# Kernel tuning notes

Measured on AMD Instinct MI355X. Metric: run time of the kernel, lower is better.

Reference implementation:

```python
import jax, jax.numpy as jnp
import numpy as np

B, H, N, C, E, D, L_OUT, LAYERS = 16, 64, 512, 3, 128, 32, 12, 2


def setup_inputs() -> dict:
    key = jax.random.key(0)
    ks = jax.random.split(key, 16)
    nrm = lambda k, s, sc=1.0: jax.random.normal(k, s, jnp.float32) * sc
    adj = jax.random.uniform(ks[0], (N, N), jnp.float32)
    adj = adj / adj.sum(axis=-1, keepdims=True)  # row-normalized prior adjacency
    return {
        "x_input": nrm(ks[1], (B, H, N, C)),
        "adj": adj,
        "Wf": nrm(ks[2], (3, E, 3 * C), 0.1),
        "Uf": nrm(ks[3], (3, E, E), 0.05),
        "bf": jnp.zeros((3, E), jnp.float32),
        "E1f": nrm(ks[4], (N, D)),
        "E2f": nrm(ks[5], (N, D)),
        "Wb": nrm(ks[6], (3, E, 3 * C), 0.1),
        "Ub": nrm(ks[7], (3, E, E), 0.05),
        "bb": jnp.zeros((3, E), jnp.float32),
        "E1b": nrm(ks[8], (N, D)),
        "E2b": nrm(ks[9], (N, D)),
        "dec_w": nrm(ks[10], (L_OUT, LAYERS, 2 * E), 0.05),  # Conv2d(layer_num->out_len, k=(1,2E)) squeezed
        "dec_b": jnp.zeros((L_OUT,), jnp.float32),
        "out_w": nrm(ks[11], (L_OUT, L_OUT), 0.1),  # 1x1 Conv2d squeezed
        "out_b": jnp.zeros((L_OUT,), jnp.float32),
    }


def _cell_step(c, xt, adj, A_dyn, W, U, b):
    # Graph-coupled GRU cell (IBNCell): xt [B,C,N], c [B,E,N].
    msg = jnp.concatenate(
        [xt,
         jnp.einsum('bcn,nm->bcm', xt, adj),      # prior-graph message passing
         jnp.einsum('bcn,nm->bcm', xt, A_dyn)],   # learned dynamic-graph message passing
        axis=1)  # [B, 3C, N]
    gx = jnp.einsum('goc,bcn->gbon', W, msg)  # 3 stacked gate projections
    r = jax.nn.sigmoid(gx[0] + jnp.einsum('oe,ben->bon', U[0], c) + b[0][:, None])
    u = jax.nn.sigmoid(gx[1] + jnp.einsum('oe,ben->bon', U[1], c) + b[1][:, None])
    g = jnp.tanh(gx[2] + jnp.einsum('oe,ben->bon', U[2], r * c) + b[2][:, None])
    return u * c + (1.0 - u) * g


def _forward(x_input, adj, Wf, Uf, bf, E1f, E2f, Wb, Ub, bb, E1b, E2b, dec_w, dec_b, out_w, out_b):
    # torch: x_input.transpose(-3,-1).transpose(-2,-1) -> [B,C,H,N]; scan layout [H,B,C,N]
    xs = jnp.transpose(x_input, (1, 0, 3, 2))
    A_f = jax.nn.softmax(jax.nn.relu(E1f @ E2f.T), axis=-1)  # dynamic adjacency, fwd cell
    A_b = jax.nn.softmax(jax.nn.relu(E1b @ E2b.T), axis=-1)  # dynamic adjacency, back cell
    c0 = jnp.zeros((xs.shape[1], Wf.shape[1], xs.shape[3]), xs.dtype)  # [B,E,N]

    def step_f(c, xt):
        cn = _cell_step(c, xt, adj, A_f, Wf, Uf, bf)
        return cn, None

    # Output only depends on the last timestep of the bidirectional concat:
    # forward branch -> final state after H steps; backward branch (after flip)
    # at t=H-1 -> its FIRST step (input x[H-1]). Dead per-step outputs elided.
    h_fwd, _ = jax.lax.scan(step_f, c0, xs)
    h_back0 = _cell_step(c0, xs[-1], adj, A_b, Wb, Ub, bb)
    last_ht = jnp.concatenate([h_fwd, h_back0], axis=1)  # [B, 2E, N]

    lt = jnp.transpose(last_ht, (0, 2, 1))  # [B, N, 2E]
    # layer loop z>0 is a no-op on current_layer_output -> final_result repeats last_ht
    final = jnp.broadcast_to(lt[:, None], (lt.shape[0], LAYERS, lt.shape[1], lt.shape[2]))
    h = jnp.einsum('blne,ole->bon', final, dec_w) + dec_b[:, None]  # decoder conv (1,2E)
    return jnp.einsum('oi,bin->bon', out_w, h) + out_b[:, None]  # 1x1 output conv -> [B,L_OUT,N]


def reference(x_input, adj, Wf, Uf, bf, E1f, E2f, Wb, Ub, bb, E1b, E2b, dec_w, dec_b, out_w, out_b):
    return _forward(x_input, adj, Wf, Uf, bf, E1f, E2f, Wb, Ub, bb, E1b, E2b, dec_w, dec_b, out_w, out_b)
```

## Files before the change

### kernel.cpp

```cpp
#include <hip/hip_runtime.h>


typedef _Float16 half8_t __attribute__((ext_vector_type(8)));
typedef __fp16 fp16x2_t __attribute__((ext_vector_type(2)));
typedef float float4_t __attribute__((ext_vector_type(4)));

#define PIN(x) asm volatile("" : "+v"(x))

__device__ __forceinline__ float exp2_(float x) { return __builtin_amdgcn_exp2f(x); }
__device__ __forceinline__ float rcp_(float x) { return __builtin_amdgcn_rcpf(x); }

__global__ __launch_bounds__(256) void prep_kernel(
    const float* __restrict__ E1f, const float* __restrict__ E2f,
    const float* __restrict__ E1b, const float* __restrict__ E2b,
    const float* __restrict__ adj, const float* __restrict__ Wf,
    const float* __restrict__ Uf, const float* __restrict__ bf,
    const float* __restrict__ Wb, const float* __restrict__ bb,
    _Float16* __restrict__ adjT, _Float16* __restrict__ AfT,
    _Float16* __restrict__ AbT, _Float16* __restrict__ ufrag,
    _Float16* __restrict__ wbfrag, _Float16* __restrict__ zpad) {
  int bid = blockIdx.x;
  int tid = threadIdx.x;
  if (bid >= 1288) {
    if (tid < 64) zpad[tid] = (_Float16)0.f;
    return;
  }
  if (bid >= 1272) {
    int r2 = bid - 1272;
    int gi = 1 + (r2 & 1);
    int og = r2 >> 1;
    float scl = (gi == 2) ? 2.8853902f : -1.4426950f;
    for (int e = tid; e < 512; e += 256) {
      int lane = e >> 3, j = e & 7;
      int o = og * 16 + (lane & 15);
      int q = (lane >> 4) * 8 + j;
      float v = (q < 9) ? Wb[gi * 1152 + o * 9 + q]
                        : (q == 9 ? bb[gi * 128 + o] : 0.f);
      wbfrag[r2 * 512 + e] = (_Float16)(v * scl);
    }
    return;
  }
  if (bid >= 1152) {
    int r = bid - 1152;
    int kb = r % 5;
    int gi = (r / 5) % 3;
    int og = r / 15;
    float scl = (gi == 2) ? 2.8853902f : -1.4426950f;
    for (int e = tid; e < 512; e += 256) {
      int lane = e >> 3, j = e & 7;
      int o = og * 16 + (lane & 15);
      int q4 = lane >> 4;
      float v;
      if (kb < 4) {
        v = Uf[gi * 16384 + o * 128 + kb * 32 + q4 * 8 + j];
      } else {
        int q = q4 * 8 + j;
        v = (q < 9) ? Wf[gi * 1152 + o * 9 + q]
                    : (q == 9 ? bf[gi * 128 + o] : 0.f);
      }
      ufrag[r * 512 + e] = (_Float16)(v * scl);
    }
    return;
  }
  if (bid >= 1024) {
    int base = (bid - 1024) * 4;
    for (int r = 0; r < 4; ++r) {
      int row = base + r;
      float v0 = adj[row * 512 + tid];
      float v1 = adj[row * 512 + tid + 256];
      adjT[(size_t)tid * 512 + row] = (_Float16)v0;
      adjT[(size_t)(tid + 256) * 512 + row] = (_Float16)v1;
    }
    return;
  }
  int which = bid >> 9;
  int row = bid & 511;
  const float* E1 = which ? E1b : E1f;
  const float* E2 = which ? E2b : E2f;
  _Float16* A = which ? AbT : AfT;
  __shared__ float e1s[32];
  __shared__ float red[256];
  if (tid < 32) e1s[tid] = E1[row * 32 + tid];
  __syncthreads();
  float s[2];
#pragma unroll
  for (int h = 0; h < 2; ++h) {
    int m = tid + h * 256;
    const float4* e2 = (const float4*)(E2 + m * 32);
    float acc = 0.f;
#pragma unroll
    for (int d4 = 0; d4 < 8; ++d4) {
      float4 v = e2[d4];
      acc = fmaf(v.x, e1s[d4 * 4 + 0], acc);
      acc = fmaf(v.y, e1s[d4 * 4 + 1], acc);
      acc = fmaf(v.z, e1s[d4 * 4 + 2], acc);
      acc = fmaf(v.w, e1s[d4 * 4 + 3], acc);
    }
    s[h] = fmaxf(acc, 0.f);
  }
  red[tid] = fmaxf(s[0], s[1]);
  __syncthreads();
  for (int off = 128; off > 0; off >>= 1) {
    if (tid < off) red[tid] = fmaxf(red[tid], red[tid + off]);
    __syncthreads();
  }
  float mx = red[0];
  __syncthreads();
  float e0 = __expf(s[0] - mx), e1v = __expf(s[1] - mx);
  red[tid] = e0 + e1v;
  __syncthreads();
  for (int off = 128; off > 0; off >>= 1) {
    if (tid < off) red[tid] += red[tid + off];
    __syncthreads();
  }
  float inv = rcp_(red[0]);
  A[(size_t)tid * 512 + row] = (_Float16)(e0 * inv);
  A[(size_t)(tid + 256) * 512 + row] = (_Float16)(e1v * inv);
}

__global__ __launch_bounds__(256, 2) void msg_kernel(
    const float* __restrict__ x, const _Float16* __restrict__ adjT,
    const _Float16* __restrict__ AfT, const _Float16* __restrict__ AbT,
    _Float16* __restrict__ msg16, _Float16* __restrict__ msgb16) {
  __shared__ __align__(16) _Float16 Alds[48 * 512];
  __shared__ __align__(16) _Float16 Sst[1024 * 16];
  int tid = threadIdx.x;
  int t = blockIdx.x >> 3;
  int n0g = (blockIdx.x & 7) * 64;
  int lane = tid & 63, og = tid >> 6;
  int l15 = lane & 15, q4 = lane >> 4, q0 = q4 * 8;
  bool is63 = (t == 63);

  {
    int b = tid >> 4, li = tid & 15;
    const float4* xb = (const float4*)(x + (size_t)(b * 64 + t) * 1536);
#pragma unroll
    for (int k = 0; k < 24; ++k) {
      float4 v = xb[k * 16 + li];
      int j0 = (k * 16 + li) * 4;
#pragma unroll
      for (int e = 0; e < 4; ++e) {
        int j = j0 + e;
        int n = (j * 21846) >> 16;
        int c = j - n * 3;
        int m = b * 3 + c;
        float val = (e == 0) ? v.x : (e == 1) ? v.y : (e == 2) ? v.z : v.w;
        Alds[m * 512 + ((((n >> 3) ^ (m & 7)) << 3) | (n & 7))] = (_Float16)val;
      }
    }
  }
  __syncthreads();

  const float4_t zero4 = {0.f, 0.f, 0.f, 0.f};
  float4_t acc[3][2], accb[3];
#pragma unroll
  for (int mt = 0; mt < 3; ++mt) { acc[mt][0] = zero4; acc[mt][1] = zero4; accb[mt] = zero4; }

  int n = n0g + og * 16 + l15;
  for (int kb = 0; kb < 16; ++kb) {
    half8_t afr[3];
#pragma unroll
    for (int mt = 0; mt < 3; ++mt) {
      int m = mt * 16 + l15;
      afr[mt] = *(const half8_t*)&Alds[m * 512 + ((((kb * 4 + q4) ^ (m & 7)) << 3))];
    }
    half8_t b0 = *(const half8_t*)&adjT[(size_t)n * 512 + kb * 32 + q0];
    half8_t b1 = *(const half8_t*)&AfT[(size_t)n * 512 + kb * 32 + q0];
#pragma unroll
    for (int mt = 0; mt < 3; ++mt) {
      acc[mt][0] = __builtin_amdgcn_mfma_f32_16x16x32_f16(afr[mt], b0, acc[mt][0], 0, 0, 0);
      acc[mt][1] = __builtin_amdgcn_mfma_f32_16x16x32_f16(afr[mt], b1, acc[mt][1], 0, 0, 0);
    }
    if (is63) {
      half8_t b2 = *(const half8_t*)&AbT[(size_t)n * 512 + kb * 32 + q0];
#pragma unroll
      for (int mt = 0; mt < 3; ++mt)
        accb[mt] = __builtin_amdgcn_mfma_f32_16x16x32_f16(afr[mt], b2, accb[mt], 0, 0, 0);
    }
  }

  for (int i = tid; i < 1024; i += 256) {
    int tb = i >> 6, nl = i & 63;
    int nn = n0g + nl;
    _Float16* row = &Sst[i * 16];
#pragma unroll
    for (int c = 0; c < 3; ++c) {
      int m = tb * 3 + c;
      row[c] = Alds[m * 512 + ((((nn >> 3) ^ (m & 7)) << 3) | (nn & 7))];
    }
    row[9] = (_Float16)1.f;
#pragma unroll
    for (int z = 10; z < 16; ++z) row[z] = (_Float16)0.f;
  }
#pragma unroll
  for (int mt = 0; mt < 3; ++mt)
#pragma unroll
    for (int r = 0; r < 4; ++r) {
      int m = mt * 16 + q4 * 4 + r;
      int tb = (m * 21846) >> 16;
      int c = m - tb * 3;
      _Float16* row = &Sst[(tb * 64 + og * 16 + l15) * 16];
      row[3 + c] = (_Float16)acc[mt][0][r];
      row[6 + c] = (_Float16)acc[mt][1][r];
    }
  __syncthreads();
  for (int i = tid; i < 2048; i += 256) {
    int rrow = i >> 1, h = i & 1;
    int tb = rrow >> 6, nl = rrow & 63;
    ((uint4*)msg16)[(((size_t)(t * 16 + tb) * 512) + n0g + nl) * 2 + h] =
        ((const uint4*)Sst)[i];
  }
  if (is63) {
    __syncthreads();
#pragma unroll
    for (int mt = 0; mt < 3; ++mt)
#pragma unroll
      for (int r = 0; r < 4; ++r) {
        int m = mt * 16 + q4 * 4 + r;
        int tb = (m * 21846) >> 16;
        int c = m - tb * 3;
        Sst[(tb * 64 + og * 16 + l15) * 16 + 6 + c] = (_Float16)accb[mt][r];
      }
    __syncthreads();
    for (int i = tid; i < 2048; i += 256) {
      int rrow = i >> 1, h = i & 1;
      int tb = rrow >> 6, nl = rrow & 63;
      ((uint4*)msgb16)[(((size_t)tb * 512) + n0g + nl) * 2 + h] =
          ((const uint4*)Sst)[i];
    }
  }
}

__global__ __launch_bounds__(512, 4) void rec_kernel(
    const _Float16* __restrict__ msg16, const _Float16* __restrict__ msgb16,
    const _Float16* __restrict__ zpad, const _Float16* __restrict__ ufrag,
    const _Float16* __restrict__ wbfrag, const float* __restrict__ dec_w,
    const float* __restrict__ dec_b, const float* __restrict__ out_w,
    const float* __restrict__ out_b, float* __restrict__ out) {
  __shared__ __align__(16) _Float16 Cbuf[2048];
  __shared__ __align__(16) _Float16 Gbuf[2048];
  __shared__ float hf_lds[128 * 16];
  __shared__ float hb_lds[128 * 16];
  __shared__ float hdec_lds[12 * 16];
  int tid = threadIdx.x, bid = blockIdx.x;
  int b = bid >> 5;
  int nt = bid & 31;
  int n0 = nt * 16;
  int lane = tid & 63, og = tid >> 6;
  int l15 = lane & 15, q4 = lane >> 4;

  half8_t afrag[3][5];
#pragma unroll
  for (int gi = 0; gi < 3; ++gi)
#pragma unroll
    for (int kb = 0; kb < 5; ++kb) {
      afrag[gi][kb] = *(const half8_t*)
          &ufrag[(size_t)(((og * 3 + gi) * 5 + kb) * 512) + lane * 8];
      PIN(afrag[gi][kb]);
    }

  if (tid < 256) {
    uint4 z; z.x = z.y = z.z = z.w = 0;
    ((uint4*)Cbuf)[tid] = z;
  }
  float cr[4] = {0.f, 0.f, 0.f, 0.f};

  const float4_t zero4 = {0.f, 0.f, 0.f, 0.f};
  union H4U { fp16x2_t h2[2]; unsigned long long u; };
  const char* base = (const char*)msg16 +
                     ((size_t)(b * 512 + n0 + l15)) * 32 + (q4 & 1) * 16;
  const char* pcur = (q4 < 2) ? base : (const char*)zpad;
  size_t tstr = (q4 < 2) ? (size_t)16 * 512 * 32 : 0;

  half8_t bm0 = *(const half8_t*)pcur;
  float4_t accr_p = __builtin_amdgcn_mfma_f32_16x16x32_f16(afrag[0][4], bm0, zero4, 0, 0, 0);
  float4_t accu_p = __builtin_amdgcn_mfma_f32_16x16x32_f16(afrag[1][4], bm0, zero4, 0, 0, 0);
  float4_t accg_p = __builtin_amdgcn_mfma_f32_16x16x32_f16(afrag[2][4], bm0, zero4, 0, 0, 0);

  int kb_w = og >> 1;
  int lane_w = ((og & 1) * 2 + (q4 >> 1)) * 16 + l15;
  int j0 = (q4 & 1) * 4;
  __syncthreads();

  for (int t = 0; t < 64; ++t) {
    const char* pnext = pcur + tstr;
    half8_t bm_n = *(const half8_t*)pnext;

    half8_t cf[4];
#pragma unroll
    for (int kb = 0; kb < 4; ++kb)
      cf[kb] = *(const half8_t*)&Cbuf[(kb * 64 + lane) * 8];

    float4_t accr = accr_p, accu = accu_p;
    __builtin_amdgcn_s_setprio(1);
#pragma unroll
    for (int kb = 0; kb < 4; ++kb) {
      accr = __builtin_amdgcn_mfma_f32_16x16x32_f16(afrag[0][kb], cf[kb], accr, 0, 0, 0);
      accu = __builtin_amdgcn_mfma_f32_16x16x32_f16(afrag[1][kb], cf[kb], accu, 0, 0, 0);
    }
    __builtin_amdgcn_s_setprio(0);

    float Eu[4];
    {
      H4U v;
#pragma unroll
      for (int r = 0; r < 2; ++r) {
        float a = rcp_(1.f + exp2_(accr[2 * r])) * cr[2 * r];
        float bq = rcp_(1.f + exp2_(accr[2 * r + 1])) * cr[2 * r + 1];
        v.h2[r] = __builtin_amdgcn_cvt_pkrtz(a, bq);
      }
      *(unsigned long long*)&Gbuf[(kb_w * 64 + lane_w) * 8 + j0] = v.u;
#pragma unroll
      for (int r = 0; r < 4; ++r) Eu[r] = exp2_(accu[r]);
    }
    __syncthreads();

    half8_t gf[4];
#pragma unroll
    for (int kb = 0; kb < 4; ++kb)
      gf[kb] = *(const half8_t*)&Gbuf[(kb * 64 + lane) * 8];
    float4_t accg = accg_p;
    __builtin_amdgcn_s_setprio(1);
#pragma unroll
    for (int kb = 0; kb < 4; ++kb)
      accg = __builtin_amdgcn_mfma_f32_16x16x32_f16(afrag[2][kb], gf[kb], accg, 0, 0, 0);
    __builtin_amdgcn_s_setprio(0);

    {
      H4U v;
      float cn[4];
#pragma unroll
      for (int r = 0; r < 4; ++r) {
        float Eg = exp2_(accg[r]);
        float d0 = Eg + 1.f;
        float den = fmaf(Eu[r], d0, d0);
        float num = fmaf(cr[r], Eg, cr[r]) + fmaf(Eu[r], Eg, -Eu[r]);
        cn[r] = num * rcp_(den);
        cr[r] = cn[r];
      }
      v.h2[0] = __builtin_amdgcn_cvt_pkrtz(cn[0], cn[1]);
      v.h2[1] = __builtin_amdgcn_cvt_pkrtz(cn[2], cn[3]);
      *(unsigned long long*)&Cbuf[(kb_w * 64 + lane_w) * 8 + j0] = v.u;
    }
    accr_p = __builtin_amdgcn_mfma_f32_16x16x32_f16(afrag[0][4], bm_n, zero4, 0, 0, 0);
    accu_p = __builtin_amdgcn_mfma_f32_16x16x32_f16(afrag[1][4], bm_n, zero4, 0, 0, 0);
    accg_p = __builtin_amdgcn_mfma_f32_16x16x32_f16(afrag[2][4], bm_n, zero4, 0, 0, 0);
    __syncthreads();
    pcur = pnext;
  }

  {
    const char* bb_base = (const char*)msgb16 +
                          ((size_t)(b * 512 + n0 + l15)) * 32 + (q4 & 1) * 16;
    const char* bp = (q4 < 2) ? bb_base : (const char*)zpad;
    half8_t bbk = *(const half8_t*)bp;
    half8_t au_f = *(const half8_t*)&wbfrag[(size_t)((og * 2 + 0) * 512) + lane * 8];
    half8_t ag_f = *(const half8_t*)&wbfrag[(size_t)((og * 2 + 1) * 512) + lane * 8];
    float4_t au = __builtin_amdgcn_mfma_f32_16x16x32_f16(au_f, bbk, zero4, 0, 0, 0);
    float4_t ag = __builtin_amdgcn_mfma_f32_16x16x32_f16(ag_f, bbk, zero4, 0, 0, 0);
#pragma unroll
    for (int r = 0; r < 4; ++r) {
      int row = og * 16 + q4 * 4 + r;
      float uu2 = rcp_(1.f + exp2_(au[r]));
      float gg = fmaf(-2.f, rcp_(exp2_(ag[r]) + 1.f), 1.f);
      hb_lds[row * 16 + l15] = (1.f - uu2) * gg;
      hf_lds[row * 16 + l15] = cr[r];
    }
  }
  __syncthreads();

  if (tid < 192) {
    int i = tid >> 4, cc = tid & 15;
    const float* dwa = dec_w + (size_t)i * 512;
    const float* dwb = dwa + 256;
    float hd = dec_b[i];
    for (int e = 0; e < 128; ++e) {
      hd = fmaf(dwa[e] + dwb[e], hf_lds[e * 16 + cc], hd);
      hd = fmaf(dwa[128 + e] + dwb[128 + e], hb_lds[e * 16 + cc], hd);
    }
    hdec_lds[i * 16 + cc] = hd;
  }
  __syncthreads();
  if (tid < 192) {
    int o = tid >> 4, cc = tid & 15;
    float v = out_b[o];
#pragma unroll
    for (int i = 0; i < 12; ++i) v = fmaf(out_w[o * 12 + i], hdec_lds[i * 16 + cc], v);
    out[((size_t)(b * 12 + o)) * 512 + n0 + cc] = v;
  }
}

extern "C" void kernel_launch(void* const* d_in, const int* in_sizes, int n_in,
                              void* d_out, int out_size, void* d_ws, size_t ws_size,
                              hipStream_t stream) {
  (void)in_sizes; (void)n_in; (void)out_size; (void)ws_size;
  const float* x     = (const float*)d_in[0];
  const float* adj   = (const float*)d_in[1];
  const float* Wf    = (const float*)d_in[2];
  const float* Uf    = (const float*)d_in[3];
  const float* bf    = (const float*)d_in[4];
  const float* E1f   = (const float*)d_in[5];
  const float* E2f   = (const float*)d_in[6];
  const float* Wb    = (const float*)d_in[7];
  const float* bb    = (const float*)d_in[9];
  const float* E1b   = (const float*)d_in[10];
  const float* E2b   = (const float*)d_in[11];
  const float* dec_w = (const float*)d_in[12];
  const float* dec_b = (const float*)d_in[13];
  const float* out_w = (const float*)d_in[14];
  const float* out_b = (const float*)d_in[15];

  _Float16* h      = (_Float16*)d_ws;
  _Float16* adjT   = h;
  _Float16* AfT    = h + 262144;
  _Float16* AbT    = h + 524288;
  _Float16* ufrag  = h + 786432;
  _Float16* wbfrag = h + 847872;
  _Float16* zpad   = h + 856064;
  _Float16* msg16  = h + 856128;
  _Float16* msgb16 = h + 9244736;

  prep_kernel<<<1289, 256, 0, stream>>>(E1f, E2f, E1b, E2b, adj, Wf, Uf, bf,
                                        Wb, bb, adjT, AfT, AbT, ufrag, wbfrag, zpad);
  msg_kernel<<<512, 256, 0, stream>>>(x, adjT, AfT, AbT, msg16, msgb16);
  rec_kernel<<<512, 512, 0, stream>>>(msg16, msgb16, zpad, ufrag, wbfrag,
                                      dec_w, dec_b, out_w, out_b, (float*)d_out);
}
```

Measured before the change: 198.4 us.

## Process two independent node tiles per block in recurrent kernel for ILP

Each rec_kernel block now handles two 16-node tiles (P and Q) at once, with duplicated LDS state buffers and interleaved MFMA chains, and the grid is halved to 256 blocks. The aim is to hide MFMA and transcendental latency in the serial 64-step recurrence by interleaving two independent dependency chains, and to amortise the per-step barriers and the register-held weight fragments over twice the work. In exchange the block count drops to 256, which on a 256-CU part leaves one block per CU, and register and LDS pressure rises (launch bounds relaxed to 2 blocks per CU). The input-projection MFMAs are also moved from the previous iteration's tail into the current step.

```diff
diff --git a/kernel.cpp b/kernel.cpp
--- a/kernel.cpp
+++ b/kernel.cpp
@@ -231,21 +231,22 @@
   }
 }
 
-__global__ __launch_bounds__(512, 4) void rec_kernel(
+__global__ __launch_bounds__(512, 2) void rec_kernel(
     const _Float16* __restrict__ msg16, const _Float16* __restrict__ msgb16,
     const _Float16* __restrict__ zpad, const _Float16* __restrict__ ufrag,
     const _Float16* __restrict__ wbfrag, const float* __restrict__ dec_w,
     const float* __restrict__ dec_b, const float* __restrict__ out_w,
     const float* __restrict__ out_b, float* __restrict__ out) {
-  __shared__ __align__(16) _Float16 Cbuf[2048];
-  __shared__ __align__(16) _Float16 Gbuf[2048];
-  __shared__ float hf_lds[128 * 16];
-  __shared__ float hb_lds[128 * 16];
-  __shared__ float hdec_lds[12 * 16];
+  __shared__ __align__(16) _Float16 CbufP[2048];
+  __shared__ __align__(16) _Float16 GbufP[2048];
+  __shared__ __align__(16) _Float16 CbufQ[2048];
+  __shared__ __align__(16) _Float16 GbufQ[2048];
+  __shared__ float hfP[128 * 16], hbP[128 * 16];
+  __shared__ float hfQ[128 * 16], hbQ[128 * 16];
+  __shared__ float hdecP[192], hdecQ[192];
   int tid = threadIdx.x, bid = blockIdx.x;
-  int b = bid >> 5;
-  int nt = bid & 31;
-  int n0 = nt * 16;
+  int b = bid >> 4;
+  int n0 = (bid & 15) * 32;
   int lane = tid & 63, og = tid >> 6;
   int l15 = lane & 15, q4 = lane >> 4;
 
@@ -259,23 +260,23 @@
       PIN(afrag[gi][kb]);
     }
 
-  if (tid < 256) {
+  {
     uint4 z; z.x = z.y = z.z = z.w = 0;
-    ((uint4*)Cbuf)[tid] = z;
-  }
-  float cr[4] = {0.f, 0.f, 0.f, 0.f};
+    if (tid < 256) ((uint4*)CbufP)[tid] = z;
+    else ((uint4*)CbufQ)[tid - 256] = z;
+  }
+  float crP[4] = {0.f, 0.f, 0.f, 0.f};
+  float crQ[4] = {0.f, 0.f, 0.f, 0.f};
 
   const float4_t zero4 = {0.f, 0.f, 0.f, 0.f};
   union H4U { fp16x2_t h2[2]; unsigned long long u; };
-  const char* base = (const char*)msg16 +
-                     ((size_t)(b * 512 + n0 + l15)) * 32 + (q4 & 1) * 16;
-  const char* pcur = (q4 < 2) ? base : (const char*)zpad;
+  const char* baseP = (const char*)msg16 +
+                      ((size_t)(b * 512 + n0 + l15)) * 32 + (q4 & 1) * 16;
+  const char* pcurP = (q4 < 2) ? baseP : (const char*)zpad;
+  const char* pcurQ = (q4 < 2) ? (baseP + 16 * 32) : (const char*)zpad;
   size_t tstr = (q4 < 2) ? (size_t)16 * 512 * 32 : 0;
-
-  half8_t bm0 = *(const half8_t*)pcur;
-  float4_t accr_p = __builtin_amdgcn_mfma_f32_16x16x32_f16(afrag[0][4], bm0, zero4, 0, 0, 0);
-  float4_t accu_p = __builtin_amdgcn_mfma_f32_16x16x32_f16(afrag[1][4], bm0, zero4, 0, 0, 0);
-  float4_t accg_p = __builtin_amdgcn_mfma_f32_16x16x32_f16(afrag[2][4], bm0, zero4, 0, 0, 0);
+  half8_t bmP = *(const half8_t*)pcurP;
+  half8_t bmQ = *(const half8_t*)pcurQ;
 
   int kb_w = og >> 1;
   int lane_w = ((og & 1) * 2 + (q4 >> 1)) * 16 + l15;
@@ -283,88 +284,132 @@
   __syncthreads();
 
   for (int t = 0; t < 64; ++t) {
-    const char* pnext = pcur + tstr;
-    half8_t bm_n = *(const half8_t*)pnext;
-
-    half8_t cf[4];
-#pragma unroll
-    for (int kb = 0; kb < 4; ++kb)
-      cf[kb] = *(const half8_t*)&Cbuf[(kb * 64 + lane) * 8];
-
-    float4_t accr = accr_p, accu = accu_p;
+    const char* pnP = pcurP + tstr;
+    const char* pnQ = pcurQ + tstr;
+    half8_t bmPn = *(const half8_t*)pnP;
+    half8_t bmQn = *(const half8_t*)pnQ;
+
+    half8_t cfP[4], cfQ[4];
+#pragma unroll
+    for (int kb = 0; kb < 4; ++kb) {
+      cfP[kb] = *(const half8_t*)&CbufP[(kb * 64 + lane) * 8];
+      cfQ[kb] = *(const half8_t*)&CbufQ[(kb * 64 + lane) * 8];
+    }
+
+    float4_t accrP = __builtin_amdgcn_mfma_f32_16x16x32_f16(afrag[0][4], bmP, zero4, 0, 0, 0);
+    float4_t accuP = __builtin_amdgcn_mfma_f32_16x16x32_f16(afrag[1][4], bmP, zero4, 0, 0, 0);
+    float4_t accrQ = __builtin_amdgcn_mfma_f32_16x16x32_f16(afrag[0][4], bmQ, zero4, 0, 0, 0);
+    float4_t accuQ = __builtin_amdgcn_mfma_f32_16x16x32_f16(afrag[1][4], bmQ, zero4, 0, 0, 0);
     __builtin_amdgcn_s_setprio(1);
 #pragma unroll
     for (int kb = 0; kb < 4; ++kb) {
-      accr = __builtin_amdgcn_mfma_f32_16x16x32_f16(afrag[0][kb], cf[kb], accr, 0, 0, 0);
-      accu = __builtin_amdgcn_mfma_f32_16x16x32_f16(afrag[1][kb], cf[kb], accu, 0, 0, 0);
+      accrP = __builtin_amdgcn_mfma_f32_16x16x32_f16(afrag[0][kb], cfP[kb], accrP, 0, 0, 0);
+      accrQ = __builtin_amdgcn_mfma_f32_16x16x32_f16(afrag[0][kb], cfQ[kb], accrQ, 0, 0, 0);
+      accuP = __builtin_amdgcn_mfma_f32_16x16x32_f16(afrag[1][kb], cfP[kb], accuP, 0, 0, 0);
+      accuQ = __builtin_amdgcn_mfma_f32_16x16x32_f16(afrag[1][kb], cfQ[kb], accuQ, 0, 0, 0);
     }
     __builtin_amdgcn_s_setprio(0);
 
-    float Eu[4];
+    float EuP[4], EuQ[4];
     {
       H4U v;
 #pragma unroll
       for (int r = 0; r < 2; ++r) {
-        float a = rcp_(1.f + exp2_(accr[2 * r])) * cr[2 * r];
-        float bq = rcp_(1.f + exp2_(accr[2 * r + 1])) * cr[2 * r + 1];
+        float a = rcp_(1.f + exp2_(accrP[2 * r])) * crP[2 * r];
+        float bq = rcp_(1.f + exp2_(accrP[2 * r + 1])) * crP[2 * r + 1];
         v.h2[r] = __builtin_amdgcn_cvt_pkrtz(a, bq);
       }
-      *(unsigned long long*)&Gbuf[(kb_w * 64 + lane_w) * 8 + j0] = v.u;
-#pragma unroll
-      for (int r = 0; r < 4; ++r) Eu[r] = exp2_(accu[r]);
-    }
-    __syncthreads();
-
-    half8_t gf[4];
-#pragma unroll
-    for (int kb = 0; kb < 4; ++kb)
-      gf[kb] = *(const half8_t*)&Gbuf[(kb * 64 + lane) * 8];
-    float4_t accg = accg_p;
+      *(unsigned long long*)&GbufP[(kb_w * 64 + lane_w) * 8 + j0] = v.u;
+      H4U w;
+#pragma unroll
+      for (int r = 0; r < 2; ++r) {
+        float a = rcp_(1.f + exp2_(accrQ[2 * r])) * crQ[2 * r];
+        float bq = rcp_(1.f + exp2_(accrQ[2 * r + 1])) * crQ[2 * r + 1];
+        w.h2[r] = __builtin_amdgcn_cvt_pkrtz(a, bq);
+      }
+      *(unsigned long long*)&GbufQ[(kb_w * 64 + lane_w) * 8 + j0] = w.u;
+#pragma unroll
+      for (int r = 0; r < 4; ++r) {
+        EuP[r] = exp2_(accuP[r]);
+        EuQ[r] = exp2_(accuQ[r]);
+      }
+    }
+    __syncthreads();
+
+    half8_t gfP[4], gfQ[4];
+#pragma unroll
+    for (int kb = 0; kb < 4; ++kb) {
+      gfP[kb] = *(const half8_t*)&GbufP[(kb * 64 + lane) * 8];
+      gfQ[kb] = *(const half8_t*)&GbufQ[(kb * 64 + lane) * 8];
+    }
+    float4_t accgP = __builtin_amdgcn_mfma_f32_16x16x32_f16(afrag[2][4], bmP, zero4, 0, 0, 0);
+    float4_t accgQ = __builtin_amdgcn_mfma_f32_16x16x32_f16(afrag[2][4], bmQ, zero4, 0, 0, 0);
     __builtin_amdgcn_s_setprio(1);
 #pragma unroll
-    for (int kb = 0; kb < 4; ++kb)
-      accg = __builtin_amdgcn_mfma_f32_16x16x32_f16(afrag[2][kb], gf[kb], accg, 0, 0, 0);
+    for (int kb = 0; kb < 4; ++kb) {
+      accgP = __builtin_amdgcn_mfma_f32_16x16x32_f16(afrag[2][kb], gfP[kb], accgP, 0, 0, 0);
+      accgQ = __builtin_amdgcn_mfma_f32_16x16x32_f16(afrag[2][kb], gfQ[kb], accgQ, 0, 0, 0);
+    }
     __builtin_amdgcn_s_setprio(0);
 
     {
       H4U v;
-      float cn[4];
+      float cnP[4], cnQ[4];
 #pragma unroll
       for (int r = 0; r < 4; ++r) {
-        float Eg = exp2_(accg[r]);
+        float Eg = exp2_(accgP[r]);
         float d0 = Eg + 1.f;
-        float den = fmaf(Eu[r], d0, d0);
-        float num = fmaf(cr[r], Eg, cr[r]) + fmaf(Eu[r], Eg, -Eu[r]);
-        cn[r] = num * rcp_(den);
-        cr[r] = cn[r];
-      }
-      v.h2[0] = __builtin_amdgcn_cvt_pkrtz(cn[0], cn[1]);
-      v.h2[1] = __builtin_amdgcn_cvt_pkrtz(cn[2], cn[3]);
-      *(unsigned long long*)&Cbuf[(kb_w * 64 + lane_w) * 8 + j0] = v.u;
-    }
-    accr_p = __builtin_amdgcn_mfma_f32_16x16x32_f16(afrag[0][4], bm_n, zero4, 0, 0, 0);
-    accu_p = __builtin_amdgcn_mfma_f32_16x16x32_f16(afrag[1][4], bm_n, zero4, 0, 0, 0);
-    accg_p = __builtin_amdgcn_mfma_f32_16x16x32_f16(afrag[2][4], bm_n, zero4, 0, 0, 0);
-    __syncthreads();
-    pcur = pnext;
+        float den = fmaf(EuP[r], d0, d0);
+        float num = fmaf(crP[r], Eg, crP[r]) + fmaf(EuP[r], Eg, -EuP[r]);
+        cnP[r] = num * rcp_(den);
+        crP[r] = cnP[r];
+      }
+      v.h2[0] = __builtin_amdgcn_cvt_pkrtz(cnP[0], cnP[1]);
+      v.h2[1] = __builtin_amdgcn_cvt_pkrtz(cnP[2], cnP[3]);
+      *(unsigned long long*)&CbufP[(kb_w * 64 + lane_w) * 8 + j0] = v.u;
+      H4U w;
+#pragma unroll
+      for (int r = 0; r < 4; ++r) {
+        float Eg = exp2_(accgQ[r]);
+        float d0 = Eg + 1.f;
+        float den = fmaf(EuQ[r], d0, d0);
+        float num = fmaf(crQ[r], Eg, crQ[r]) + fmaf(EuQ[r], Eg, -EuQ[r]);
+        cnQ[r] = num * rcp_(den);
+        crQ[r] = cnQ[r];
+      }
+      w.h2[0] = __builtin_amdgcn_cvt_pkrtz(cnQ[0], cnQ[1]);
+      w.h2[1] = __builtin_amdgcn_cvt_pkrtz(cnQ[2], cnQ[3]);
+      *(unsigned long long*)&CbufQ[(kb_w * 64 + lane_w) * 8 + j0] = w.u;
+    }
+    __syncthreads();
+    bmP = bmPn; bmQ = bmQn;
+    pcurP = pnP; pcurQ = pnQ;
   }
 
   {
-    const char* bb_base = (const char*)msgb16 +
-                          ((size_t)(b * 512 + n0 + l15)) * 32 + (q4 & 1) * 16;
-    const char* bp = (q4 < 2) ? bb_base : (const char*)zpad;
-    half8_t bbk = *(const half8_t*)bp;
+    const char* bbP = (const char*)msgb16 +
+                      ((size_t)(b * 512 + n0 + l15)) * 32 + (q4 & 1) * 16;
+    const char* bpP = (q4 < 2) ? bbP : (const char*)zpad;
+    const char* bpQ = (q4 < 2) ? (bbP + 16 * 32) : (const char*)zpad;
+    half8_t bkP = *(const half8_t*)bpP;
+    half8_t bkQ = *(const half8_t*)bpQ;
     half8_t au_f = *(const half8_t*)&wbfrag[(size_t)((og * 2 + 0) * 512) + lane * 8];
     half8_t ag_f = *(const half8_t*)&wbfrag[(size_t)((og * 2 + 1) * 512) + lane * 8];
-    float4_t au = __builtin_amdgcn_mfma_f32_16x16x32_f16(au_f, bbk, zero4, 0, 0, 0);
-    float4_t ag = __builtin_amdgcn_mfma_f32_16x16x32_f16(ag_f, bbk, zero4, 0, 0, 0);
+    float4_t auP = __builtin_amdgcn_mfma_f32_16x16x32_f16(au_f, bkP, zero4, 0, 0, 0);
+    float4_t agP = __builtin_amdgcn_mfma_f32_16x16x32_f16(ag_f, bkP, zero4, 0, 0, 0);
+    float4_t auQ = __builtin_amdgcn_mfma_f32_16x16x32_f16(au_f, bkQ, zero4, 0, 0, 0);
+    float4_t agQ = __builtin_amdgcn_mfma_f32_16x16x32_f16(ag_f, bkQ, zero4, 0, 0, 0);
 #pragma unroll
     for (int r = 0; r < 4; ++r) {
       int row = og * 16 + q4 * 4 + r;
-      float uu2 = rcp_(1.f + exp2_(au[r]));
-      float gg = fmaf(-2.f, rcp_(exp2_(ag[r]) + 1.f), 1.f);
-      hb_lds[row * 16 + l15] = (1.f - uu2) * gg;
-      hf_lds[row * 16 + l15] = cr[r];
+      float uuP = rcp_(1.f + exp2_(auP[r]));
+      float ggP = fmaf(-2.f, rcp_(exp2_(agP[r]) + 1.f), 1.f);
+      hbP[row * 16 + l15] = (1.f - uuP) * ggP;
+      hfP[row * 16 + l15] = crP[r];
+      float uuQ = rcp_(1.f + exp2_(auQ[r]));
+      float ggQ = fmaf(-2.f, rcp_(exp2_(agQ[r]) + 1.f), 1.f);
+      hbQ[row * 16 + l15] = (1.f - uuQ) * ggQ;
+      hfQ[row * 16 + l15] = crQ[r];
     }
   }
   __syncthreads();
@@ -375,18 +420,36 @@
     const float* dwb = dwa + 256;
     float hd = dec_b[i];
     for (int e = 0; e < 128; ++e) {
-      hd = fmaf(dwa[e] + dwb[e], hf_lds[e * 16 + cc], hd);
-      hd = fmaf(dwa[128 + e] + dwb[128 + e], hb_lds[e * 16 + cc], hd);
-    }
-    hdec_lds[i * 16 + cc] = hd;
+      hd = fmaf(dwa[e] + dwb[e], hfP[e * 16 + cc], hd);
+      hd = fmaf(dwa[128 + e] + dwb[128 + e], hbP[e * 16 + cc], hd);
+    }
+    hdecP[i * 16 + cc] = hd;
+  } else if (tid >= 256 && tid < 448) {
+    int t2 = tid - 256;
+    int i = t2 >> 4, cc = t2 & 15;
+    const float* dwa = dec_w + (size_t)i * 512;
+    const float* dwb = dwa + 256;
+    float hd = dec_b[i];
+    for (int e = 0; e < 128; ++e) {
+      hd = fmaf(dwa[e] + dwb[e], hfQ[e * 16 + cc], hd);
+      hd = fmaf(dwa[128 + e] + dwb[128 + e], hbQ[e * 16 + cc], hd);
+    }
+    hdecQ[i * 16 + cc] = hd;
   }
   __syncthreads();
   if (tid < 192) {
     int o = tid >> 4, cc = tid & 15;
     float v = out_b[o];
 #pragma unroll
-    for (int i = 0; i < 12; ++i) v = fmaf(out_w[o * 12 + i], hdec_lds[i * 16 + cc], v);
+    for (int i = 0; i < 12; ++i) v = fmaf(out_w[o * 12 + i], hdecP[i * 16 + cc], v);
     out[((size_t)(b * 12 + o)) * 512 + n0 + cc] = v;
+  } else if (tid >= 256 && tid < 448) {
+    int t2 = tid - 256;
+    int o = t2 >> 4, cc = t2 & 15;
+    float v = out_b[o];
+#pragma unroll
+    for (int i = 0; i < 12; ++i) v = fmaf(out_w[o * 12 + i], hdecQ[i * 16 + cc], v);
+    out[((size_t)(b * 12 + o)) * 512 + n0 + 16 + cc] = v;
   }
 }
 
@@ -423,6 +486,6 @@
   prep_kernel<<<1289, 256, 0, stream>>>(E1f, E2f, E1b, E2b, adj, Wf, Uf, bf,
                                         Wb, bb, adjT, AfT, AbT, ufrag, wbfrag, zpad);
   msg_kernel<<<512, 256, 0, stream>>>(x, adjT, AfT, AbT, msg16, msgb16);
-  rec_kernel<<<512, 512, 0, stream>>>(msg16, msgb16, zpad, ufrag, wbfrag,
+  rec_kernel<<<256, 512, 0, stream>>>(msg16, msgb16, zpad, ufrag, wbfrag,
                                       dec_w, dec_b, out_w, out_b, (float*)d_out);
 }
```

New measurement: 209.0 us. +5.4%, slower.

## Halve rec_kernel waves so each wave computes two interleaved gate row tiles

Applied to the files above, without the earlier changes.

The recurrent kernel now runs 4 waves of 256 threads instead of 8. Each wave owns two 16-row output tiles and interleaves their independent MFMA chains, which is meant to hide MFMA latency and make the per-step barriers cheaper. The input-projection MFMAs are no longer precomputed for the next step; they now start each step's accumulation. That adds work on the serial critical path and roughly doubles the VGPRs pinned for weight fragments.

```diff
diff --git a/kernel.cpp b/kernel.cpp
--- a/kernel.cpp
+++ b/kernel.cpp
@@ -231,7 +231,7 @@
   }
 }
 
-__global__ __launch_bounds__(512, 4) void rec_kernel(
+__global__ __launch_bounds__(256, 2) void rec_kernel(
     const _Float16* __restrict__ msg16, const _Float16* __restrict__ msgb16,
     const _Float16* __restrict__ zpad, const _Float16* __restrict__ ufrag,
     const _Float16* __restrict__ wbfrag, const float* __restrict__ dec_w,
@@ -249,21 +249,23 @@
   int lane = tid & 63, og = tid >> 6;
   int l15 = lane & 15, q4 = lane >> 4;
 
-  half8_t afrag[3][5];
-#pragma unroll
-  for (int gi = 0; gi < 3; ++gi)
-#pragma unroll
-    for (int kb = 0; kb < 5; ++kb) {
-      afrag[gi][kb] = *(const half8_t*)
-          &ufrag[(size_t)(((og * 3 + gi) * 5 + kb) * 512) + lane * 8];
-      PIN(afrag[gi][kb]);
-    }
-
-  if (tid < 256) {
+  half8_t afrag[2][3][5];
+#pragma unroll
+  for (int h = 0; h < 2; ++h)
+#pragma unroll
+    for (int gi = 0; gi < 3; ++gi)
+#pragma unroll
+      for (int kb = 0; kb < 5; ++kb) {
+        afrag[h][gi][kb] = *(const half8_t*)
+            &ufrag[(size_t)((((og * 2 + h) * 3 + gi) * 5 + kb) * 512) + lane * 8];
+        PIN(afrag[h][gi][kb]);
+      }
+
+  {
     uint4 z; z.x = z.y = z.z = z.w = 0;
     ((uint4*)Cbuf)[tid] = z;
   }
-  float cr[4] = {0.f, 0.f, 0.f, 0.f};
+  float cr[2][4] = {{0.f, 0.f, 0.f, 0.f}, {0.f, 0.f, 0.f, 0.f}};
 
   const float4_t zero4 = {0.f, 0.f, 0.f, 0.f};
   union H4U { fp16x2_t h2[2]; unsigned long long u; };
@@ -271,15 +273,10 @@
                      ((size_t)(b * 512 + n0 + l15)) * 32 + (q4 & 1) * 16;
   const char* pcur = (q4 < 2) ? base : (const char*)zpad;
   size_t tstr = (q4 < 2) ? (size_t)16 * 512 * 32 : 0;
-
-  half8_t bm0 = *(const half8_t*)pcur;
-  float4_t accr_p = __builtin_amdgcn_mfma_f32_16x16x32_f16(afrag[0][4], bm0, zero4, 0, 0, 0);
-  float4_t accu_p = __builtin_amdgcn_mfma_f32_16x16x32_f16(afrag[1][4], bm0, zero4, 0, 0, 0);
-  float4_t accg_p = __builtin_amdgcn_mfma_f32_16x16x32_f16(afrag[2][4], bm0, zero4, 0, 0, 0);
-
-  int kb_w = og >> 1;
-  int lane_w = ((og & 1) * 2 + (q4 >> 1)) * 16 + l15;
+  half8_t bm = *(const half8_t*)pcur;
+
   int j0 = (q4 & 1) * 4;
+  int lwbase = (q4 >> 1) * 16 + l15;
   __syncthreads();
 
   for (int t = 0; t < 64; ++t) {
@@ -291,27 +288,35 @@
     for (int kb = 0; kb < 4; ++kb)
       cf[kb] = *(const half8_t*)&Cbuf[(kb * 64 + lane) * 8];
 
-    float4_t accr = accr_p, accu = accu_p;
+    float4_t accr[2], accu[2];
     __builtin_amdgcn_s_setprio(1);
 #pragma unroll
-    for (int kb = 0; kb < 4; ++kb) {
-      accr = __builtin_amdgcn_mfma_f32_16x16x32_f16(afrag[0][kb], cf[kb], accr, 0, 0, 0);
-      accu = __builtin_amdgcn_mfma_f32_16x16x32_f16(afrag[1][kb], cf[kb], accu, 0, 0, 0);
-    }
+    for (int h = 0; h < 2; ++h) {
+      accr[h] = __builtin_amdgcn_mfma_f32_16x16x32_f16(afrag[h][0][4], bm, zero4, 0, 0, 0);
+      accu[h] = __builtin_amdgcn_mfma_f32_16x16x32_f16(afrag[h][1][4], bm, zero4, 0, 0, 0);
+    }
+#pragma unroll
+    for (int kb = 0; kb < 4; ++kb)
+#pragma unroll
+      for (int h = 0; h < 2; ++h) {
+        accr[h] = __builtin_amdgcn_mfma_f32_16x16x32_f16(afrag[h][0][kb], cf[kb], accr[h], 0, 0, 0);
+        accu[h] = __builtin_amdgcn_mfma_f32_16x16x32_f16(afrag[h][1][kb], cf[kb], accu[h], 0, 0, 0);
+      }
     __builtin_amdgcn_s_setprio(0);
 
-    float Eu[4];
-    {
+    float Eu[2][4];
+#pragma unroll
+    for (int h = 0; h < 2; ++h) {
       H4U v;
 #pragma unroll
       for (int r = 0; r < 2; ++r) {
-        float a = rcp_(1.f + exp2_(accr[2 * r])) * cr[2 * r];
-        float bq = rcp_(1.f + exp2_(accr[2 * r + 1])) * cr[2 * r + 1];
+        float a = rcp_(1.f + exp2_(accr[h][2 * r])) * cr[h][2 * r];
+        float bq = rcp_(1.f + exp2_(accr[h][2 * r + 1])) * cr[h][2 * r + 1];
         v.h2[r] = __builtin_amdgcn_cvt_pkrtz(a, bq);
       }
-      *(unsigned long long*)&Gbuf[(kb_w * 64 + lane_w) * 8 + j0] = v.u;
-#pragma unroll
-      for (int r = 0; r < 4; ++r) Eu[r] = exp2_(accu[r]);
+      *(unsigned long long*)&Gbuf[(og * 64 + h * 32 + lwbase) * 8 + j0] = v.u;
+#pragma unroll
+      for (int r = 0; r < 4; ++r) Eu[h][r] = exp2_(accu[h][r]);
     }
     __syncthreads();
 
@@ -319,33 +324,37 @@
 #pragma unroll
     for (int kb = 0; kb < 4; ++kb)
       gf[kb] = *(const half8_t*)&Gbuf[(kb * 64 + lane) * 8];
-    float4_t accg = accg_p;
+    float4_t accg[2];
     __builtin_amdgcn_s_setprio(1);
 #pragma unroll
+    for (int h = 0; h < 2; ++h)
+      accg[h] = __builtin_amdgcn_mfma_f32_16x16x32_f16(afrag[h][2][4], bm, zero4, 0, 0, 0);
+#pragma unroll
     for (int kb = 0; kb < 4; ++kb)
-      accg = __builtin_amdgcn_mfma_f32_16x16x32_f16(afrag[2][kb], gf[kb], accg, 0, 0, 0);
+#pragma unroll
+      for (int h = 0; h < 2; ++h)
+        accg[h] = __builtin_amdgcn_mfma_f32_16x16x32_f16(afrag[h][2][kb], gf[kb], accg[h], 0, 0, 0);
     __builtin_amdgcn_s_setprio(0);
 
-    {
+#pragma unroll
+    for (int h = 0; h < 2; ++h) {
       H4U v;
       float cn[4];
 #pragma unroll
       for (int r = 0; r < 4; ++r) {
-        float Eg = exp2_(accg[r]);
+        float Eg = exp2_(accg[h][r]);
         float d0 = Eg + 1.f;
-        float den = fmaf(Eu[r], d0, d0);
-        float num = fmaf(cr[r], Eg, cr[r]) + fmaf(Eu[r], Eg, -Eu[r]);
+        float den = fmaf(Eu[h][r], d0, d0);
+        float num = fmaf(cr[h][r], Eg, cr[h][r]) + fmaf(Eu[h][r], Eg, -Eu[h][r]);
         cn[r] = num * rcp_(den);
-        cr[r] = cn[r];
+        cr[h][r] = cn[r];
       }
       v.h2[0] = __builtin_amdgcn_cvt_pkrtz(cn[0], cn[1]);
       v.h2[1] = __builtin_amdgcn_cvt_pkrtz(cn[2], cn[3]);
-      *(unsigned long long*)&Cbuf[(kb_w * 64 + lane_w) * 8 + j0] = v.u;
-    }
-    accr_p = __builtin_amdgcn_mfma_f32_16x16x32_f16(afrag[0][4], bm_n, zero4, 0, 0, 0);
-    accu_p = __builtin_amdgcn_mfma_f32_16x16x32_f16(afrag[1][4], bm_n, zero4, 0, 0, 0);
-    accg_p = __builtin_amdgcn_mfma_f32_16x16x32_f16(afrag[2][4], bm_n, zero4, 0, 0, 0);
-    __syncthreads();
+      *(unsigned long long*)&Cbuf[(og * 64 + h * 32 + lwbase) * 8 + j0] = v.u;
+    }
+    __syncthreads();
+    bm = bm_n;
     pcur = pnext;
   }
 
@@ -354,17 +363,21 @@
                           ((size_t)(b * 512 + n0 + l15)) * 32 + (q4 & 1) * 16;
     const char* bp = (q4 < 2) ? bb_base : (const char*)zpad;
     half8_t bbk = *(const half8_t*)bp;
-    half8_t au_f = *(const half8_t*)&wbfrag[(size_t)((og * 2 + 0) * 512) + lane * 8];
-    half8_t ag_f = *(const half8_t*)&wbfrag[(size_t)((og * 2 + 1) * 512) + lane * 8];
-    float4_t au = __builtin_amdgcn_mfma_f32_16x16x32_f16(au_f, bbk, zero4, 0, 0, 0);
-    float4_t ag = __builtin_amdgcn_mfma_f32_16x16x32_f16(ag_f, bbk, zero4, 0, 0, 0);
-#pragma unroll
-    for (int r = 0; r < 4; ++r) {
-      int row = og * 16 + q4 * 4 + r;
-      float uu2 = rcp_(1.f + exp2_(au[r]));
-      float gg = fmaf(-2.f, rcp_(exp2_(ag[r]) + 1.f), 1.f);
-      hb_lds[row * 16 + l15] = (1.f - uu2) * gg;
-      hf_lds[row * 16 + l15] = cr[r];
+#pragma unroll
+    for (int h = 0; h < 2; ++h) {
+      int oo = og * 2 + h;
+      half8_t au_f = *(const half8_t*)&wbfrag[(size_t)((oo * 2 + 0) * 512) + lane * 8];
+      half8_t ag_f = *(const half8_t*)&wbfrag[(size_t)((oo * 2 + 1) * 512) + lane * 8];
+      float4_t au = __builtin_amdgcn_mfma_f32_16x16x32_f16(au_f, bbk, zero4, 0, 0, 0);
+      float4_t ag = __builtin_amdgcn_mfma_f32_16x16x32_f16(ag_f, bbk, zero4, 0, 0, 0);
+#pragma unroll
+      for (int r = 0; r < 4; ++r) {
+        int row = oo * 16 + q4 * 4 + r;
+        float uu2 = rcp_(1.f + exp2_(au[r]));
+        float gg = fmaf(-2.f, rcp_(exp2_(ag[r]) + 1.f), 1.f);
+        hb_lds[row * 16 + l15] = (1.f - uu2) * gg;
+        hf_lds[row * 16 + l15] = cr[h][r];
+      }
     }
   }
   __syncthreads();
@@ -423,6 +436,6 @@
   prep_kernel<<<1289, 256, 0, stream>>>(E1f, E2f, E1b, E2b, adj, Wf, Uf, bf,
                                         Wb, bb, adjT, AfT, AbT, ufrag, wbfrag, zpad);
   msg_kernel<<<512, 256, 0, stream>>>(x, adjT, AfT, AbT, msg16, msgb16);
-  rec_kernel<<<512, 512, 0, stream>>>(msg16, msgb16, zpad, ufrag, wbfrag,
+  rec_kernel<<<512, 256, 0, stream>>>(msg16, msgb16, zpad, ufrag, wbfrag,
                                       dec_w, dec_b, out_w, out_b, (float*)d_out);
 }
```

Result: slower. 203.7 us (+2.7%).

## Move update-gate MFMAs off the critical path and vectorize x staging

Applied to the files above, without the earlier changes.

In the recurrent scan, the update-gate (u) matmul and its input projection now run after the first barrier, alongside the candidate-gate MFMAs, so only the reset gate sits before the first synchronization. The intent is to shorten the serialized path between the C load and the G write and barrier. In exchange the phase after the barrier carries more MFMA work and bm must stay live across iterations. Separately, msg_kernel's x staging now loads 24 contiguous floats per thread, packs them to fp16 pairs and writes 16-byte LDS stores instead of scalar half stores with divide-by-3 indexing.

```diff
diff --git a/kernel.cpp b/kernel.cpp
--- a/kernel.cpp
+++ b/kernel.cpp
@@ -132,20 +132,24 @@
   bool is63 = (t == 63);
 
   {
-    int b = tid >> 4, li = tid & 15;
-    const float4* xb = (const float4*)(x + (size_t)(b * 64 + t) * 1536);
-#pragma unroll
-    for (int k = 0; k < 24; ++k) {
-      float4 v = xb[k * 16 + li];
-      int j0 = (k * 16 + li) * 4;
-#pragma unroll
-      for (int e = 0; e < 4; ++e) {
-        int j = j0 + e;
-        int n = (j * 21846) >> 16;
-        int c = j - n * 3;
+    union F24 { float4 v4[6]; float f[24]; };
+    union P16 { fp16x2_t h2[4]; uint4 u; };
+#pragma unroll
+    for (int it = 0; it < 4; ++it) {
+      int task = tid + it * 256;
+      int b = task >> 6, chunk = task & 63;
+      F24 fv;
+      const float4* xb4 = (const float4*)x + ((size_t)(b * 64 + t) * 384 + chunk * 6);
+#pragma unroll
+      for (int i = 0; i < 6; ++i) fv.v4[i] = xb4[i];
+#pragma unroll
+      for (int c = 0; c < 3; ++c) {
+        P16 p;
+#pragma unroll
+        for (int i = 0; i < 4; ++i)
+          p.h2[i] = __builtin_amdgcn_cvt_pkrtz(fv.f[6 * i + c], fv.f[6 * i + 3 + c]);
         int m = b * 3 + c;
-        float val = (e == 0) ? v.x : (e == 1) ? v.y : (e == 2) ? v.z : v.w;
-        Alds[m * 512 + ((((n >> 3) ^ (m & 7)) << 3) | (n & 7))] = (_Float16)val;
+        *(uint4*)&Alds[m * 512 + ((chunk ^ (m & 7)) << 3)] = p.u;
       }
     }
   }
@@ -271,11 +275,9 @@
                      ((size_t)(b * 512 + n0 + l15)) * 32 + (q4 & 1) * 16;
   const char* pcur = (q4 < 2) ? base : (const char*)zpad;
   size_t tstr = (q4 < 2) ? (size_t)16 * 512 * 32 : 0;
-
-  half8_t bm0 = *(const half8_t*)pcur;
-  float4_t accr_p = __builtin_amdgcn_mfma_f32_16x16x32_f16(afrag[0][4], bm0, zero4, 0, 0, 0);
-  float4_t accu_p = __builtin_amdgcn_mfma_f32_16x16x32_f16(afrag[1][4], bm0, zero4, 0, 0, 0);
-  float4_t accg_p = __builtin_amdgcn_mfma_f32_16x16x32_f16(afrag[2][4], bm0, zero4, 0, 0, 0);
+  half8_t bm = *(const half8_t*)pcur;
+
+  float4_t accr_p = __builtin_amdgcn_mfma_f32_16x16x32_f16(afrag[0][4], bm, zero4, 0, 0, 0);
 
   int kb_w = og >> 1;
   int lane_w = ((og & 1) * 2 + (q4 >> 1)) * 16 + l15;
@@ -291,16 +293,13 @@
     for (int kb = 0; kb < 4; ++kb)
       cf[kb] = *(const half8_t*)&Cbuf[(kb * 64 + lane) * 8];
 
-    float4_t accr = accr_p, accu = accu_p;
+    float4_t accr = accr_p;
     __builtin_amdgcn_s_setprio(1);
 #pragma unroll
-    for (int kb = 0; kb < 4; ++kb) {
+    for (int kb = 0; kb < 4; ++kb)
       accr = __builtin_amdgcn_mfma_f32_16x16x32_f16(afrag[0][kb], cf[kb], accr, 0, 0, 0);
-      accu = __builtin_amdgcn_mfma_f32_16x16x32_f16(afrag[1][kb], cf[kb], accu, 0, 0, 0);
-    }
     __builtin_amdgcn_s_setprio(0);
 
-    float Eu[4];
     {
       H4U v;
 #pragma unroll
@@ -310,8 +309,6 @@
         v.h2[r] = __builtin_amdgcn_cvt_pkrtz(a, bq);
       }
       *(unsigned long long*)&Gbuf[(kb_w * 64 + lane_w) * 8 + j0] = v.u;
-#pragma unroll
-      for (int r = 0; r < 4; ++r) Eu[r] = exp2_(accu[r]);
     }
     __syncthreads();
 
@@ -319,8 +316,12 @@
 #pragma unroll
     for (int kb = 0; kb < 4; ++kb)
       gf[kb] = *(const half8_t*)&Gbuf[(kb * 64 + lane) * 8];
-    float4_t accg = accg_p;
     __builtin_amdgcn_s_setprio(1);
+    float4_t accu = __builtin_amdgcn_mfma_f32_16x16x32_f16(afrag[1][4], bm, zero4, 0, 0, 0);
+#pragma unroll
+    for (int kb = 0; kb < 4; ++kb)
+      accu = __builtin_amdgcn_mfma_f32_16x16x32_f16(afrag[1][kb], cf[kb], accu, 0, 0, 0);
+    float4_t accg = __builtin_amdgcn_mfma_f32_16x16x32_f16(afrag[2][4], bm, zero4, 0, 0, 0);
 #pragma unroll
     for (int kb = 0; kb < 4; ++kb)
       accg = __builtin_amdgcn_mfma_f32_16x16x32_f16(afrag[2][kb], gf[kb], accg, 0, 0, 0);
@@ -331,10 +332,11 @@
       float cn[4];
 #pragma unroll
       for (int r = 0; r < 4; ++r) {
+        float Eu = exp2_(accu[r]);
         float Eg = exp2_(accg[r]);
         float d0 = Eg + 1.f;
-        float den = fmaf(Eu[r], d0, d0);
-        float num = fmaf(cr[r], Eg, cr[r]) + fmaf(Eu[r], Eg, -Eu[r]);
+        float den = fmaf(Eu, d0, d0);
+        float num = fmaf(cr[r], Eg, cr[r]) + fmaf(Eu, Eg, -Eu);
         cn[r] = num * rcp_(den);
         cr[r] = cn[r];
       }
@@ -343,9 +345,8 @@
       *(unsigned long long*)&Cbuf[(kb_w * 64 + lane_w) * 8 + j0] = v.u;
     }
     accr_p = __builtin_amdgcn_mfma_f32_16x16x32_f16(afrag[0][4], bm_n, zero4, 0, 0, 0);
-    accu_p = __builtin_amdgcn_mfma_f32_16x16x32_f16(afrag[1][4], bm_n, zero4, 0, 0, 0);
-    accg_p = __builtin_amdgcn_mfma_f32_16x16x32_f16(afrag[2][4], bm_n, zero4, 0, 0, 0);
-    __syncthreads();
+    __syncthreads();
+    bm = bm_n;
     pcur = pnext;
   }
 
```

New measurement: 195.6 us (median of 2 runs). No clear change (-1.4%).
